# Optimization experiments

Hardware: AMD Instinct MI355X
Metric: run time of the kernel (lower is better)

Reference implementation:

```python
import jax, jax.numpy as jnp
import numpy as np

B, DEPTH, X, H, C = 512, 9, 128, 64, 16
NPT = 2 ** (DEPTH + 1) - 1  # 1023 nodes per perfect binary tree (heap layout)


def setup_inputs() -> dict:
    key = jax.random.key(0)
    ks = jax.random.split(key, 5)
    s = 0.05
    return {
        "embeddings": jax.random.normal(ks[0], (B, NPT, X), jnp.float32),
        "h0": jnp.zeros((B, NPT, H), jnp.float32),
        "c0": jnp.zeros((B, NPT, H), jnp.float32),
        "W_iou": jax.random.normal(ks[1], (X, 3 * H), jnp.float32) * s,
        "U_iou": jax.random.normal(ks[2], (2 * H, 3 * H), jnp.float32) * s,
        "b_iou": jnp.zeros((3 * H,), jnp.float32),
        "Uf_w": jax.random.normal(ks[3], (2 * H, 2 * H), jnp.float32) * s,
        "Uf_b": jnp.zeros((2 * H,), jnp.float32),
        "lin_w": jax.random.normal(ks[4], (H, C), jnp.float32) * s,
        "lin_b": jnp.zeros((C,), jnp.float32),
    }


def _apply_gates(iou, c_base):
    # apply_node_func: i,o,u chunks -> c = sig(i)*tanh(u) + c_base; h = sig(o)*tanh(c)
    i, o, u = jnp.split(iou, 3, axis=-1)
    c = jax.nn.sigmoid(i) * jnp.tanh(u) + c_base
    h = jax.nn.sigmoid(o) * jnp.tanh(c)
    return h, c


def reference(embeddings, h0, c0, W_iou, U_iou, b_iou, Uf_w, Uf_b, lin_w, lin_b):
    h, c = h0, c0
    # --- leaves (no in-edges): iou = W_iou(x) + b_iou, c_base = initial c ---
    ls = 2 ** DEPTH - 1  # first leaf index
    iou = embeddings[:, ls:] @ W_iou + b_iou
    hl, cl = _apply_gates(iou, c0[:, ls:])
    h = h.at[:, ls:].set(hl)
    c = c.at[:, ls:].set(cl)
    # --- internal levels, deepest -> root (topological propagation) ---
    for lvl in range(DEPTH - 1, -1, -1):
        s0, n = 2 ** lvl - 1, 2 ** lvl
        # children of nodes [s0, s0+n) are the contiguous block [2*s0+1, 2*s0+1+2n)
        cs = 2 * s0 + 1
        hc = h[:, cs:cs + 2 * n].reshape(B, n, 2 * H)   # h_cat = [h_left, h_right]
        cc = c[:, cs:cs + 2 * n].reshape(B, n, 2, H)
        # reduce_func: f = sigmoid(U_f(h_cat)); c_red = sum(f * c_children)
        f = jax.nn.sigmoid(hc @ Uf_w.T + Uf_b).reshape(B, n, 2, H)
        c_red = jnp.sum(f * cc, axis=2)
        # DGL overwrite semantics: internal iou = U_iou(h_cat) (+ b_iou in apply)
        iou = hc @ U_iou + b_iou
        hn, cn = _apply_gates(iou, c_red)
        h = h.at[:, s0:s0 + n].set(hn)
        c = c.at[:, s0:s0 + n].set(cn)
    # global mean pool over nodes per tree, then classifier + softmax
    hm = jnp.mean(h, axis=1)  # [B, H]
    logits = hm @ lin_w + lin_b
    return jax.nn.softmax(logits, axis=-1)
```

## Files before the change

kernel.cpp:

```cpp
#include <hip/hip_runtime.h>
#include <hip/hip_bf16.h>
#include <stdint.h>

#define NPT 1023
#define LEAF_TILES 12
#define INT_TILES  20

typedef float f32x4 __attribute__((ext_vector_type(4)));
typedef __bf16 bf16x8_t __attribute__((ext_vector_type(8)));

__device__ __forceinline__ unsigned int f32_to_bf16(float f) {
    unsigned int u = __float_as_uint(f);
    u += 0x7FFFu + ((u >> 16) & 1u);
    return u >> 16;
}
__device__ __forceinline__ float bf16_ld(const void* p) {
    return __uint_as_float(((unsigned int)*(const unsigned short*)p) << 16);
}
__device__ __forceinline__ float sigm(float x) {
    return __builtin_amdgcn_rcpf(1.0f + __expf(-x));
}
__device__ __forceinline__ float tanh_f(float x) {
    return 1.0f - 2.0f * __builtin_amdgcn_rcpf(1.0f + __expf(2.0f * x));
}
__device__ __forceinline__ f32x4 mfma16(uint4 a, uint4 b, f32x4 c) {
    return __builtin_amdgcn_mfma_f32_16x16x32_bf16(
        __builtin_bit_cast(bf16x8_t, a), __builtin_bit_cast(bf16x8_t, b), c, 0, 0, 0);
}

__global__ void prep_kernel(const float* __restrict__ W_iou,
                            const float* __restrict__ U_iou,
                            const float* __restrict__ Uf_w,
                            unsigned short* __restrict__ leafB,
                            unsigned short* __restrict__ intB) {
    int tid = blockIdx.x * blockDim.x + threadIdx.x;
    const int leaf_slots = LEAF_TILES * 4 * 64;
    const int total = (LEAF_TILES + INT_TILES) * 4 * 64;
    if (tid >= total) return;
    bool leaf = tid < leaf_slots;
    int s = leaf ? tid : tid - leaf_slots;
    int tile = s >> 8;
    int ks = (s >> 6) & 3;
    int l = s & 63;
    int col = tile * 16 + (l & 15);
    int k0 = ks * 32 + (l >> 4) * 8;
    unsigned short vals[8];
#pragma unroll
    for (int i = 0; i < 8; ++i) {
        int k = k0 + i;
        float v;
        if (leaf) v = W_iou[k * 192 + col];
        else      v = (col < 192) ? U_iou[k * 192 + col]
                                  : Uf_w[(col - 192) * 128 + k];
        vals[i] = (unsigned short)f32_to_bf16(v);
    }
    uint4* dst = (uint4*)(leaf ? leafB : intB);
    dst[s] = *(const uint4*)vals;
}

__global__ __launch_bounds__(256, 3) void mega_kernel(
        const float* __restrict__ emb,
        float* __restrict__ hbuf,
        float* __restrict__ cbuf,
        const unsigned short* __restrict__ leafB,
        const unsigned short* __restrict__ intB,
        const float* __restrict__ b_iou,
        const float* __restrict__ Uf_b) {
    __shared__ __align__(16) unsigned char cw[32768];
    __shared__ __align__(16) unsigned char hB[16384];

    const int tid = threadIdx.x;
    const int t = blockIdx.x >> 2, e = blockIdx.x & 3;
    const int wave = tid >> 6, lane = tid & 63;
    const int lrow = lane & 15, kgrp = lane >> 4;
    const int c = wave * 16 + lrow;

    const uint4* BfL = (const uint4*)leafB;
    uint4 BL[12];
#pragma unroll
    for (int nt = 0; nt < 3; ++nt)
#pragma unroll
        for (int ks = 0; ks < 4; ++ks)
            BL[nt * 4 + ks] = BfL[((wave + 4 * nt) * 4 + ks) * 64 + lane];

    const float* embBase = emb + ((size_t)(t * NPT + 511 + 128 * e)) * 128;
#pragma unroll
    for (int it = 0; it < 8; ++it) {
        int qid = it * 256 + tid;
        int r = qid >> 4, j = qid & 15;
        const float* s = embBase + r * 128 + j * 8;
        float4 v0 = *(const float4*)s;
        float4 v1 = *(const float4*)(s + 4);
        uint4 pk;
        pk.x = f32_to_bf16(v0.x) | (f32_to_bf16(v0.y) << 16);
        pk.y = f32_to_bf16(v0.z) | (f32_to_bf16(v0.w) << 16);
        pk.z = f32_to_bf16(v1.x) | (f32_to_bf16(v1.y) << 16);
        pk.w = f32_to_bf16(v1.z) | (f32_to_bf16(v1.w) << 16);
        *(uint4*)&cw[r * 256 + ((j ^ (r & 15)) << 4)] = pk;
    }
    __syncthreads();

    const float bi = b_iou[c], bo = b_iou[64 + c], bu = b_iou[128 + c];
    const float bfl = Uf_b[c], bfr = Uf_b[64 + c];
    float psum = 0.f;

#pragma unroll
    for (int p = 0; p < 2; ++p) {
        f32x4 acc[4][3];
#pragma unroll
        for (int mt = 0; mt < 4; ++mt)
#pragma unroll
            for (int nt = 0; nt < 3; ++nt)
                acc[mt][nt] = (f32x4){0.f, 0.f, 0.f, 0.f};
#pragma unroll
        for (int mt = 0; mt < 4; ++mt) {
            const int row = p * 64 + mt * 16 + lrow;
            uint4 A[4];
#pragma unroll
            for (int ks = 0; ks < 4; ++ks)
                A[ks] = *(const uint4*)&cw[row * 256 + (((4 * ks + kgrp) ^ (row & 15)) << 4)];
#pragma unroll
            for (int nt = 0; nt < 3; ++nt)
#pragma unroll
                for (int ks = 0; ks < 4; ++ks)
                    acc[mt][nt] = mfma16(A[ks], BL[nt * 4 + ks], acc[mt][nt]);
        }
        if (p == 0) __syncthreads();
#pragma unroll
        for (int mt = 0; mt < 4; ++mt)
#pragma unroll
            for (int q = 0; q < 4; ++q) {
                const int row = p * 64 + mt * 16 + kgrp * 4 + q;
                float i_ = acc[mt][0][q] + bi;
                float o_ = acc[mt][1][q] + bo;
                float u_ = acc[mt][2][q] + bu;
                float cn = sigm(i_) * tanh_f(u_);
                float hn = sigm(o_) * tanh_f(cn);
                psum += hn;
                *(unsigned short*)&cw[(row * 64 + c) * 2] = (unsigned short)f32_to_bf16(cn);
                *(unsigned short*)&hB[row * 128 + (((c >> 3) ^ ((row >> 1) & 7)) << 4) + (c & 7) * 2] =
                    (unsigned short)f32_to_bf16(hn);
            }
    }

    const uint4* BfI = (const uint4*)intB;
    uint4 BI[20];
#pragma unroll
    for (int nt = 0; nt < 5; ++nt)
#pragma unroll
        for (int ks = 0; ks < 4; ++ks)
            BI[nt * 4 + ks] = BfI[((wave + 4 * nt) * 4 + ks) * 64 + lane];
    __syncthreads();

#pragma unroll
    for (int p = 0; p < 2; ++p) {
        f32x4 acc2[2][5];
#pragma unroll
        for (int mt = 0; mt < 2; ++mt)
#pragma unroll
            for (int nt = 0; nt < 5; ++nt)
                acc2[mt][nt] = (f32x4){0.f, 0.f, 0.f, 0.f};
#pragma unroll
        for (int mt = 0; mt < 2; ++mt) {
            const int row = p * 32 + mt * 16 + lrow;
            uint4 A[4];
#pragma unroll
            for (int ks = 0; ks < 4; ++ks) {
                const int n = 2 * row + (ks >> 1);
                A[ks] = *(const uint4*)&hB[n * 128 + ((((ks & 1) * 4 + kgrp) ^ (row & 7)) << 4)];
            }
#pragma unroll
            for (int nt = 0; nt < 5; ++nt)
#pragma unroll
                for (int ks = 0; ks < 4; ++ks)
                    acc2[mt][nt] = mfma16(A[ks], BI[nt * 4 + ks], acc2[mt][nt]);
        }
        if (p == 0) __syncthreads();
        float* cPar = (float*)(cw + 16384);
#pragma unroll
        for (int mt = 0; mt < 2; ++mt)
#pragma unroll
            for (int q = 0; q < 4; ++q) {
                const int row = p * 32 + mt * 16 + kgrp * 4 + q;
                float cl = bf16_ld(&cw[((2 * row) * 64 + c) * 2]);
                float cr = bf16_ld(&cw[((2 * row + 1) * 64 + c) * 2]);
                float i_ = acc2[mt][0][q] + bi;
                float o_ = acc2[mt][1][q] + bo;
                float u_ = acc2[mt][2][q] + bu;
                float fl = sigm(acc2[mt][3][q] + bfl);
                float fr = sigm(acc2[mt][4][q] + bfr);
                float cn = sigm(i_) * tanh_f(u_) + fl * cl + fr * cr;
                float hn = sigm(o_) * tanh_f(cn);
                psum += hn;
                cPar[row * 64 + c] = cn;
                *(unsigned short*)&hB[row * 128 + (((c >> 3) ^ ((row >> 1) & 7)) << 4) + (c & 7) * 2] =
                    (unsigned short)f32_to_bf16(hn);
            }
    }
    __syncthreads();

    for (int lvl = 2; lvl <= 7; ++lvl) {
        const int M = 128 >> lvl;
        const int MT = (M + 15) >> 4;
        f32x4 acc2[2][5];
#pragma unroll
        for (int mt = 0; mt < 2; ++mt)
#pragma unroll
            for (int nt = 0; nt < 5; ++nt)
                acc2[mt][nt] = (f32x4){0.f, 0.f, 0.f, 0.f};
#pragma unroll
        for (int mt = 0; mt < 2; ++mt) if (mt < MT) {
            const int row = mt * 16 + lrow;
            uint4 A[4];
#pragma unroll
            for (int ks = 0; ks < 4; ++ks) {
                const int n = 2 * row + (ks >> 1);
                A[ks] = *(const uint4*)&hB[n * 128 + ((((ks & 1) * 4 + kgrp) ^ (row & 7)) << 4)];
            }
#pragma unroll
            for (int nt = 0; nt < 5; ++nt)
#pragma unroll
                for (int ks = 0; ks < 4; ++ks)
                    acc2[mt][nt] = mfma16(A[ks], BI[nt * 4 + ks], acc2[mt][nt]);
        }
        __syncthreads();
        const float* cChild = (const float*)(cw + ((lvl & 1) ? 0 : 16384));
        float* cPar = (float*)(cw + ((lvl & 1) ? 16384 : 0));
#pragma unroll
        for (int mt = 0; mt < 2; ++mt) if (mt < MT)
#pragma unroll
            for (int q = 0; q < 4; ++q) {
                const int row = mt * 16 + kgrp * 4 + q;
                if (row < M) {
                    float cl = cChild[(2 * row) * 64 + c];
                    float cr = cChild[(2 * row + 1) * 64 + c];
                    float i_ = acc2[mt][0][q] + bi;
                    float o_ = acc2[mt][1][q] + bo;
                    float u_ = acc2[mt][2][q] + bu;
                    float fl = sigm(acc2[mt][3][q] + bfl);
                    float fr = sigm(acc2[mt][4][q] + bfr);
                    float cn = sigm(i_) * tanh_f(u_) + fl * cl + fr * cr;
                    float hn = sigm(o_) * tanh_f(cn);
                    psum += hn;
                    if (lvl < 7) {
                        cPar[row * 64 + c] = cn;
                        *(unsigned short*)&hB[row * 128 + (((c >> 3) ^ ((row >> 1) & 7)) << 4) + (c & 7) * 2] =
                            (unsigned short)f32_to_bf16(hn);
                    } else {
                        size_t gi = ((size_t)(t * NPT + 3 + e)) * 64 + c;
                        hbuf[gi] = hn;
                        cbuf[gi] = cn;
                    }
                }
            }
        __syncthreads();
    }

    psum += __shfl_xor(psum, 16);
    psum += __shfl_xor(psum, 32);
    if (kgrp == 0)
        hbuf[((size_t)(t * NPT + 8 + e)) * 64 + c] = psum;
}

__global__ __launch_bounds__(256) void final_kernel(
        float* __restrict__ hbuf,
        const float* __restrict__ cbuf,
        const unsigned short* __restrict__ intB,
        const float* __restrict__ b_iou,
        const float* __restrict__ Uf_b,
        const float* __restrict__ lin_w,
        const float* __restrict__ lin_b,
        float* __restrict__ out) {
    __shared__ unsigned short hc1[16][128];
    __shared__ unsigned short hc0[16][128];
    __shared__ float sc[4][64];
    __shared__ float c12[2][64];
    __shared__ float hm[64];

    const int tid = threadIdx.x;
    const int t = blockIdx.x;
    const int wave = tid >> 6, lane = tid & 63;
    const int lrow = lane & 15, kgrp = lane >> 4;
    const int c = wave * 16 + lrow;

    {
        const int nd = tid >> 6, col = tid & 63;
        size_t gi = ((size_t)(t * NPT + 3 + nd)) * 64 + col;
        float hv = hbuf[gi];
        sc[nd][col] = cbuf[gi];
        hc1[nd >> 1][(nd & 1) * 64 + col] = (unsigned short)f32_to_bf16(hv);
    }
    const uint4* BfI = (const uint4*)intB;
    uint4 BI[20];
#pragma unroll
    for (int nt = 0; nt < 5; ++nt)
#pragma unroll
        for (int ks = 0; ks < 4; ++ks)
            BI[nt * 4 + ks] = BfI[((wave + 4 * nt) * 4 + ks) * 64 + lane];
    __syncthreads();

    const float bi = b_iou[c], bo = b_iou[64 + c], bu = b_iou[128 + c];
    const float bfl = Uf_b[c], bfr = Uf_b[64 + c];
    float psum = 0.f;

    f32x4 a1[5];
#pragma unroll
    for (int nt = 0; nt < 5; ++nt) a1[nt] = (f32x4){0.f, 0.f, 0.f, 0.f};
#pragma unroll
    for (int ks = 0; ks < 4; ++ks) {
        uint4 A = *(const uint4*)&hc1[lrow][ks * 32 + kgrp * 8];
#pragma unroll
        for (int nt = 0; nt < 5; ++nt) a1[nt] = mfma16(A, BI[nt * 4 + ks], a1[nt]);
    }
#pragma unroll
    for (int q = 0; q < 4; ++q) {
        const int row = kgrp * 4 + q;
        if (row < 2) {
            float cl = sc[2 * row][c];
            float cr = sc[2 * row + 1][c];
            float i_ = a1[0][q] + bi, o_ = a1[1][q] + bo, u_ = a1[2][q] + bu;
            float fl = sigm(a1[3][q] + bfl), fr = sigm(a1[4][q] + bfr);
            float cn = sigm(i_) * tanh_f(u_) + fl * cl + fr * cr;
            float hn = sigm(o_) * tanh_f(cn);
            psum += hn;
            c12[row][c] = cn;
            hc0[0][row * 64 + c] = (unsigned short)f32_to_bf16(hn);
        }
    }
    __syncthreads();

    f32x4 a0[5];
#pragma unroll
    for (int nt = 0; nt < 5; ++nt) a0[nt] = (f32x4){0.f, 0.f, 0.f, 0.f};
#pragma unroll
    for (int ks = 0; ks < 4; ++ks) {
        uint4 A = *(const uint4*)&hc0[lrow][ks * 32 + kgrp * 8];
#pragma unroll
        for (int nt = 0; nt < 5; ++nt) a0[nt] = mfma16(A, BI[nt * 4 + ks], a0[nt]);
    }
    if (kgrp == 0) {
        float cl = c12[0][c], cr = c12[1][c];
        float i_ = a0[0][0] + bi, o_ = a0[1][0] + bo, u_ = a0[2][0] + bu;
        float fl = sigm(a0[3][0] + bfl), fr = sigm(a0[4][0] + bfr);
        float cn = sigm(i_) * tanh_f(u_) + fl * cl + fr * cr;
        float hn = sigm(o_) * tanh_f(cn);
        psum += hn;
    }

    psum += __shfl_xor(psum, 16);
    psum += __shfl_xor(psum, 32);
    if (kgrp == 0) hm[c] = psum;
    __syncthreads();
    if (tid < 64) {
        float s = hm[tid];
#pragma unroll
        for (int e2 = 0; e2 < 4; ++e2)
            s += hbuf[((size_t)(t * NPT + 8 + e2)) * 64 + tid];
        hm[tid] = s * (1.0f / 1023.0f);
    }
    __syncthreads();
    if (tid < 16) {
        int cc = tid;
        float lg = lin_b[cc];
#pragma unroll
        for (int dd = 0; dd < 64; ++dd) lg += hm[dd] * lin_w[dd * 16 + cc];
        float mx = lg;
#pragma unroll
        for (int off = 8; off; off >>= 1) mx = fmaxf(mx, __shfl_xor(mx, off, 16));
        float ex = expf(lg - mx);
        float sm = ex;
#pragma unroll
        for (int off = 8; off; off >>= 1) sm += __shfl_xor(sm, off, 16);
        out[t * 16 + cc] = ex / sm;
    }
}

extern "C" void kernel_launch(void* const* d_in, const int* in_sizes, int n_in,
                              void* d_out, int out_size, void* d_ws, size_t ws_size,
                              hipStream_t stream) {
    const float* emb   = (const float*)d_in[0];
    float*       hbuf  = (float*)d_in[1];
    float*       cbuf  = (float*)d_in[2];
    const float* W_iou = (const float*)d_in[3];
    const float* U_iou = (const float*)d_in[4];
    const float* b_iou = (const float*)d_in[5];
    const float* Uf_w  = (const float*)d_in[6];
    const float* Uf_b  = (const float*)d_in[7];
    const float* lin_w = (const float*)d_in[8];
    const float* lin_b = (const float*)d_in[9];
    float* out = (float*)d_out;

    unsigned short* leafB = (unsigned short*)d_ws;
    unsigned short* intB  = leafB + (size_t)LEAF_TILES * 4 * 64 * 8;

    prep_kernel<<<32, 256, 0, stream>>>(W_iou, U_iou, Uf_w, leafB, intB);
    mega_kernel<<<2048, 256, 0, stream>>>(emb, hbuf, cbuf, leafB, intB, b_iou, Uf_b);
    final_kernel<<<512, 256, 0, stream>>>(hbuf, cbuf, intB, b_iou, Uf_b, lin_w, lin_b, out);
}
```

Before: 507.7 us.

## Double-buffer LDS h/c state to drop per-level barriers in tree kernel

Adds separate LDS buffers for leaf c values and ping-pong h buffers so each level reads children from one buffer and writes parents to another. This removes the mid-level __syncthreads and lets the leaf and first internal levels run as single passes with larger accumulator arrays. The cost is more LDS (about 72KB per block) and more registers, so launch bounds drop from 3 to 2 blocks per CU, which lowers occupancy.

```diff
diff --git a/kernel.cpp b/kernel.cpp
--- a/kernel.cpp
+++ b/kernel.cpp
@@ -14,8 +14,8 @@
     u += 0x7FFFu + ((u >> 16) & 1u);
     return u >> 16;
 }
-__device__ __forceinline__ float bf16_ld(const void* p) {
-    return __uint_as_float(((unsigned int)*(const unsigned short*)p) << 16);
+__device__ __forceinline__ float bf16_ld(const unsigned short* p) {
+    return __uint_as_float(((unsigned int)*p) << 16);
 }
 __device__ __forceinline__ float sigm(float x) {
     return __builtin_amdgcn_rcpf(1.0f + __expf(-x));
@@ -58,7 +58,7 @@
     dst[s] = *(const uint4*)vals;
 }
 
-__global__ __launch_bounds__(256, 3) void mega_kernel(
+__global__ __launch_bounds__(256, 2) void mega_kernel(
         const float* __restrict__ emb,
         float* __restrict__ hbuf,
         float* __restrict__ cbuf,
@@ -67,7 +67,8 @@
         const float* __restrict__ b_iou,
         const float* __restrict__ Uf_b) {
     __shared__ __align__(16) unsigned char cw[32768];
-    __shared__ __align__(16) unsigned char hB[16384];
+    __shared__ __align__(16) unsigned short leafC[8192];
+    __shared__ __align__(16) unsigned char hB[24576];
 
     const int tid = threadIdx.x;
     const int t = blockIdx.x >> 2, e = blockIdx.x & 3;
@@ -104,17 +105,16 @@
     const float bfl = Uf_b[c], bfr = Uf_b[64 + c];
     float psum = 0.f;
 
-#pragma unroll
-    for (int p = 0; p < 2; ++p) {
-        f32x4 acc[4][3];
-#pragma unroll
-        for (int mt = 0; mt < 4; ++mt)
+    {
+        f32x4 acc[8][3];
+#pragma unroll
+        for (int mt = 0; mt < 8; ++mt)
 #pragma unroll
             for (int nt = 0; nt < 3; ++nt)
                 acc[mt][nt] = (f32x4){0.f, 0.f, 0.f, 0.f};
 #pragma unroll
-        for (int mt = 0; mt < 4; ++mt) {
-            const int row = p * 64 + mt * 16 + lrow;
+        for (int mt = 0; mt < 8; ++mt) {
+            const int row = mt * 16 + lrow;
             uint4 A[4];
 #pragma unroll
             for (int ks = 0; ks < 4; ++ks)
@@ -125,19 +125,18 @@
                 for (int ks = 0; ks < 4; ++ks)
                     acc[mt][nt] = mfma16(A[ks], BL[nt * 4 + ks], acc[mt][nt]);
         }
-        if (p == 0) __syncthreads();
-#pragma unroll
-        for (int mt = 0; mt < 4; ++mt)
+#pragma unroll
+        for (int mt = 0; mt < 8; ++mt)
 #pragma unroll
             for (int q = 0; q < 4; ++q) {
-                const int row = p * 64 + mt * 16 + kgrp * 4 + q;
+                const int row = mt * 16 + kgrp * 4 + q;
                 float i_ = acc[mt][0][q] + bi;
                 float o_ = acc[mt][1][q] + bo;
                 float u_ = acc[mt][2][q] + bu;
                 float cn = sigm(i_) * tanh_f(u_);
                 float hn = sigm(o_) * tanh_f(cn);
                 psum += hn;
-                *(unsigned short*)&cw[(row * 64 + c) * 2] = (unsigned short)f32_to_bf16(cn);
+                leafC[row * 64 + c] = (unsigned short)f32_to_bf16(cn);
                 *(unsigned short*)&hB[row * 128 + (((c >> 3) ^ ((row >> 1) & 7)) << 4) + (c & 7) * 2] =
                     (unsigned short)f32_to_bf16(hn);
             }
@@ -152,17 +151,16 @@
             BI[nt * 4 + ks] = BfI[((wave + 4 * nt) * 4 + ks) * 64 + lane];
     __syncthreads();
 
-#pragma unroll
-    for (int p = 0; p < 2; ++p) {
-        f32x4 acc2[2][5];
-#pragma unroll
-        for (int mt = 0; mt < 2; ++mt)
+    {
+        f32x4 acc2[4][5];
+#pragma unroll
+        for (int mt = 0; mt < 4; ++mt)
 #pragma unroll
             for (int nt = 0; nt < 5; ++nt)
                 acc2[mt][nt] = (f32x4){0.f, 0.f, 0.f, 0.f};
 #pragma unroll
-        for (int mt = 0; mt < 2; ++mt) {
-            const int row = p * 32 + mt * 16 + lrow;
+        for (int mt = 0; mt < 4; ++mt) {
+            const int row = mt * 16 + lrow;
             uint4 A[4];
 #pragma unroll
             for (int ks = 0; ks < 4; ++ks) {
@@ -175,15 +173,14 @@
                 for (int ks = 0; ks < 4; ++ks)
                     acc2[mt][nt] = mfma16(A[ks], BI[nt * 4 + ks], acc2[mt][nt]);
         }
-        if (p == 0) __syncthreads();
         float* cPar = (float*)(cw + 16384);
 #pragma unroll
-        for (int mt = 0; mt < 2; ++mt)
+        for (int mt = 0; mt < 4; ++mt)
 #pragma unroll
             for (int q = 0; q < 4; ++q) {
-                const int row = p * 32 + mt * 16 + kgrp * 4 + q;
-                float cl = bf16_ld(&cw[((2 * row) * 64 + c) * 2]);
-                float cr = bf16_ld(&cw[((2 * row + 1) * 64 + c) * 2]);
+                const int row = mt * 16 + kgrp * 4 + q;
+                float cl = bf16_ld(&leafC[(2 * row) * 64 + c]);
+                float cr = bf16_ld(&leafC[(2 * row + 1) * 64 + c]);
                 float i_ = acc2[mt][0][q] + bi;
                 float o_ = acc2[mt][1][q] + bo;
                 float u_ = acc2[mt][2][q] + bu;
@@ -193,7 +190,7 @@
                 float hn = sigm(o_) * tanh_f(cn);
                 psum += hn;
                 cPar[row * 64 + c] = cn;
-                *(unsigned short*)&hB[row * 128 + (((c >> 3) ^ ((row >> 1) & 7)) << 4) + (c & 7) * 2] =
+                *(unsigned short*)&hB[16384 + row * 128 + (((c >> 3) ^ ((row >> 1) & 7)) << 4) + (c & 7) * 2] =
                     (unsigned short)f32_to_bf16(hn);
             }
     }
@@ -202,6 +199,10 @@
     for (int lvl = 2; lvl <= 7; ++lvl) {
         const int M = 128 >> lvl;
         const int MT = (M + 15) >> 4;
+        const unsigned char* hChild = (lvl & 1) ? hB : hB + 16384;
+        unsigned char* hPar = (lvl & 1) ? hB + 16384 : hB;
+        const float* cChild = (const float*)((lvl & 1) ? cw : cw + 16384);
+        float* cPar = (float*)((lvl & 1) ? cw + 16384 : cw);
         f32x4 acc2[2][5];
 #pragma unroll
         for (int mt = 0; mt < 2; ++mt)
@@ -215,7 +216,7 @@
 #pragma unroll
             for (int ks = 0; ks < 4; ++ks) {
                 const int n = 2 * row + (ks >> 1);
-                A[ks] = *(const uint4*)&hB[n * 128 + ((((ks & 1) * 4 + kgrp) ^ (row & 7)) << 4)];
+                A[ks] = *(const uint4*)&hChild[n * 128 + ((((ks & 1) * 4 + kgrp) ^ (row & 7)) << 4)];
             }
 #pragma unroll
             for (int nt = 0; nt < 5; ++nt)
@@ -223,9 +224,6 @@
                 for (int ks = 0; ks < 4; ++ks)
                     acc2[mt][nt] = mfma16(A[ks], BI[nt * 4 + ks], acc2[mt][nt]);
         }
-        __syncthreads();
-        const float* cChild = (const float*)(cw + ((lvl & 1) ? 0 : 16384));
-        float* cPar = (float*)(cw + ((lvl & 1) ? 16384 : 0));
 #pragma unroll
         for (int mt = 0; mt < 2; ++mt) if (mt < MT)
 #pragma unroll
@@ -244,7 +242,7 @@
                     psum += hn;
                     if (lvl < 7) {
                         cPar[row * 64 + c] = cn;
-                        *(unsigned short*)&hB[row * 128 + (((c >> 3) ^ ((row >> 1) & 7)) << 4) + (c & 7) * 2] =
+                        *(unsigned short*)&hPar[row * 128 + (((c >> 3) ^ ((row >> 1) & 7)) << 4) + (c & 7) * 2] =
                             (unsigned short)f32_to_bf16(hn);
                     } else {
                         size_t gi = ((size_t)(t * NPT + 3 + e)) * 64 + c;
@@ -253,7 +251,7 @@
                     }
                 }
             }
-        __syncthreads();
+        if (lvl < 7) __syncthreads();
     }
 
     psum += __shfl_xor(psum, 16);
```

Measured after the change: 494.9 us. -2.5%, faster.
